# Optimization experiments

Hardware: AMD Instinct MI355X
Metric: run time of the kernel (lower is better)

The kernel has to match this reference:

```python
import jax, jax.numpy as jnp
import numpy as np

B, V, T, F = 1, 16, 1, 1
ZF, ZA, ZQ = 5, 4, 7
N = 12 * 4 ** ZF          # 12288 field nodes
n = 4 ** (ZQ - ZF)        # 16 packed channels per node (in_features_q)
K = 9                     # adjc.shape[-1], neighborhood size
ATT = 128                 # att_dim
H = 32                    # n_head_channels
NH = ATT // H             # 4 heads
NA = 4 ** (ZF - ZA)       # 4-node local attention window
MULT = 2


def _ln(x, s, b):
    m = jnp.mean(x, axis=-1, keepdims=True)
    v = jnp.mean((x - m) ** 2, axis=-1, keepdims=True)
    return (x - m) * jax.lax.rsqrt(v + 1e-5) * s + b


def setup_inputs() -> dict:
    key = jax.random.key(0)
    ks = jax.random.split(key, 8)
    d = {}
    d["x"] = jax.random.normal(ks[0], (B, V, T, N * n, F), jnp.float32)
    d["adjc"] = jax.random.randint(ks[1], (N, K), 0, N)
    d["ln1_scale"] = jnp.ones((n,), jnp.float32)
    d["ln1_bias"] = jnp.zeros((n,), jnp.float32)
    d["W_q"] = jax.random.normal(ks[2], (n, ATT), jnp.float32) / np.sqrt(n)
    d["W_kv"] = jax.random.normal(ks[3], (n * K, 2 * ATT), jnp.float32) / np.sqrt(n * K)
    d["b_kv"] = jnp.zeros((2 * ATT,), jnp.float32)
    d["W_out"] = jax.random.normal(ks[4], (ATT, n), jnp.float32) / np.sqrt(ATT)
    d["b_out"] = jnp.zeros((n,), jnp.float32)
    d["gamma"] = jnp.full((n,), 1e-6, jnp.float32)
    d["ln2_scale"] = jnp.ones((n,), jnp.float32)
    d["ln2_bias"] = jnp.zeros((n,), jnp.float32)
    d["W1"] = jax.random.normal(ks[5], (n, n * MULT), jnp.float32) / np.sqrt(n)
    d["b1"] = jnp.zeros((n * MULT,), jnp.float32)
    d["W2"] = jax.random.normal(ks[6], (n * MULT, n), jnp.float32) / np.sqrt(n * MULT)
    d["b2"] = jnp.zeros((n,), jnp.float32)
    d["gamma_mlp"] = jnp.full((n,), 1e-6, jnp.float32)
    return d


def _forward(x, adjc, ln1_scale, ln1_bias, W_q, W_kv, b_kv, W_out, b_out,
             gamma, ln2_scale, ln2_bias, W1, b1, W2, b2, gamma_mlp):
    fv = F * V
    Ng = N // NA
    # combine_zooms + 'b v t N n f -> b (f v) t N n'
    xc = x.reshape(B, V, T, N, n, F)
    q = jnp.transpose(xc, (0, 5, 1, 2, 3, 4)).reshape(B, fv, T, N, n)
    x_res = q
    # emb_layer_q: layer norm, identity linear (in == out features)
    q = _ln(q, ln1_scale, ln1_bias)
    kv = q  # self-attention: kv shares the normalized q
    # q projection (no bias) and local-window reshape
    qp = (q @ W_q).reshape(B, fv, T, Ng, NA, ATT)
    # neighborhood gather on kv (with_nh_field): [b,fv,t,N,K,n] -> [b,fv,t,N,K*n]
    kv_nh = kv[:, :, :, adjc, :].reshape(B, fv, T, N, K * n)
    kvp = (kv_nh @ W_kv + b_kv).reshape(B, fv, T, Ng, NA, 2 * ATT)
    k, v = jnp.split(kvp, 2, axis=-1)

    def to_att(z):
        # 'b fv t N NA (NH H) -> (b N t) NH (fv NA) H'  (with_var_att)
        z = z.reshape(B, fv, T, Ng, NA, NH, H)
        z = jnp.transpose(z, (0, 3, 2, 5, 1, 4, 6))
        return z.reshape(B * Ng * T, NH, fv * NA, H)

    qa, ka, va = to_att(qp), to_att(k), to_att(v)
    scores = jnp.einsum('znqh,znkh->znqk', qa, ka) / jnp.sqrt(jnp.asarray(H, qa.dtype))
    att = jax.nn.softmax(scores, axis=-1)
    out = jnp.einsum('znqk,znkh->znqh', att, va)
    # '(b N t) NH (fv NA) H -> b fv t (N NA) (NH H)'
    out = out.reshape(B, Ng, T, NH, fv, NA, H)
    out = jnp.transpose(out, (0, 4, 2, 1, 5, 3, 6)).reshape(B, fv, T, Ng * NA, NH * H)
    att_out = out @ W_out + b_out           # [b,fv,t,N,n]
    xo = x_res + gamma * att_out            # 'shift' update with gamma residual
    h = _ln(xo, ln2_scale, ln2_bias)        # mlp_emb_layer (identity linear)
    mlp = jax.nn.gelu(h @ W1 + b1) @ W2 + b2
    xo = xo + gamma_mlp * mlp
    # 'b (f v) t N n -> b v t (N n) f'
    y = xo.reshape(B, F, V, T, N, n)
    y = jnp.transpose(y, (0, 2, 3, 4, 5, 1)).reshape(B, V, T, N * n, F)
    return y


def reference(x, adjc, ln1_scale, ln1_bias, W_q, W_kv, b_kv, W_out, b_out,
              gamma, ln2_scale, ln2_bias, W1, b1, W2, b2, gamma_mlp):
    return _forward(x, adjc, ln1_scale, ln1_bias, W_q, W_kv, b_kv, W_out, b_out,
                    gamma, ln2_scale, ln2_bias, W1, b1, W2, b2, gamma_mlp)
```

## Files before the change

kernel.cpp:

```cpp
#include <hip/hip_runtime.h>
#include <math.h>

#define NNODE 12288
#define XSTRIDE 196608
#define NGRP 3072
#define XT_ELEMS 3145728
#define WS_WQT   0
#define WS_WKVT  4096
#define WS_WOUTT 45056
#define WS_W1T   47104
#define WS_W2T   48128
#define WS_WTOT  48640
#define WS_BYTES ((size_t)(XT_ELEMS + WS_WTOT) * 2)

typedef unsigned short u16;
typedef short short8 __attribute__((ext_vector_type(8)));
typedef float f32x4 __attribute__((ext_vector_type(4)));

#define MFMA16(a,b,c) __builtin_amdgcn_mfma_f32_16x16x32_bf16((a),(b),(c),0,0,0)

__device__ __forceinline__ u16 f2b(float f) {
  unsigned u = __float_as_uint(f);
  return (u16)((u + 0x7FFFu + ((u >> 16) & 1u)) >> 16);
}
__device__ __forceinline__ unsigned pk2(float a, float b) {
  return (__float_as_uint(a) >> 16) | (__float_as_uint(b) & 0xFFFF0000u);
}
__device__ __forceinline__ float gelu_fast(float v) {
  float u = v * (1.0f + 0.044715f * v * v);
  float e = __expf(-1.5957691216057308f * u);
  return v / (1.0f + e);
}
#define DS_FENCE() do { asm volatile("s_waitcnt lgkmcnt(0)" ::: "memory"); \
                        __builtin_amdgcn_sched_barrier(0); } while (0)

__device__ __forceinline__ float softmax16(f32x4 s4[4]) {
  const float C2 = 0.25508682300212037f;
  f32x4 m01, m23;
  #pragma unroll
  for (int r = 0; r < 4; ++r) { m01[r] = fmaxf(s4[0][r], s4[1][r]); m23[r] = fmaxf(s4[2][r], s4[3][r]); }
  float mx = fmaxf(fmaxf(fmaxf(m01[0], m23[0]), fmaxf(m01[1], m23[1])),
                   fmaxf(fmaxf(m01[2], m23[2]), fmaxf(m01[3], m23[3])));
  mx = fmaxf(mx, __shfl_xor(mx, 16));
  mx = fmaxf(mx, __shfl_xor(mx, 32));
  float nmx = mx * C2;
  float sum = 0.f;
  #pragma unroll
  for (int mt = 0; mt < 4; ++mt)
    #pragma unroll
    for (int r = 0; r < 4; ++r) {
      float e = exp2f(__builtin_fmaf(s4[mt][r], C2, -nmx));
      s4[mt][r] = e; sum += e;
    }
  sum += __shfl_xor(sum, 16);
  sum += __shfl_xor(sum, 32);
  return 1.0f / sum;
}

__global__ __launch_bounds__(256)
void ln1x_prep(const float* __restrict__ x, const float* __restrict__ ln1s,
               const float* __restrict__ ln1b,
               const float* __restrict__ Wq, const float* __restrict__ Wkv,
               const float* __restrict__ Wout, const float* __restrict__ W1,
               const float* __restrict__ W2, u16* __restrict__ ws)
{
  const int t = threadIdx.x;
  if (blockIdx.x >= 768) {
    int i = (blockIdx.x - 768) * 256 + t;
    if (i >= WS_WTOT) return;
    u16* wbase = ws + XT_ELEMS;
    int j = i;
    if (j < 4096)  { int n = j >> 5, k = j & 31;   wbase[WS_WQT   + j] = f2b(k < 16  ? Wq[k * 128 + n]  : 0.f); return; }
    j -= 4096;
    if (j < 40960) { int n = j / 160, k = j % 160; wbase[WS_WKVT  + j] = f2b(k < 144 ? Wkv[k * 256 + n] : 0.f); return; }
    j -= 40960;
    if (j < 2048)  { int n = j >> 7, k = j & 127;  wbase[WS_WOUTT + j] = f2b(Wout[k * 16 + n]); return; }
    j -= 2048;
    if (j < 1024)  { int n = j >> 5, k = j & 31;   wbase[WS_W1T   + j] = f2b(k < 16 ? W1[k * 32 + n] : 0.f); return; }
    j -= 1024;
    { int n = j >> 5, k = j & 31; wbase[WS_W2T + j] = f2b(W2[k * 16 + n]); }
    return;
  }
  __shared__ u16 buf[4096];
  const int node0 = blockIdx.x * 16;
  const int v = t >> 4, nd = t & 15;
  const f32x4* xp = (const f32x4*)(x + (size_t)v * XSTRIDE + (node0 + nd) * 16);
  f32x4 p0 = xp[0], p1 = xp[1], p2 = xp[2], p3 = xp[3];
  float va[16] = {p0[0],p0[1],p0[2],p0[3], p1[0],p1[1],p1[2],p1[3],
                  p2[0],p2[1],p2[2],p2[3], p3[0],p3[1],p3[2],p3[3]};
  float s = 0.f, ss = 0.f;
  #pragma unroll
  for (int j = 0; j < 16; ++j) { s += va[j]; ss += va[j] * va[j]; }
  float mean = s * 0.0625f, rs = rsqrtf(ss * 0.0625f - mean * mean + 1e-5f);
  short8 o0, o1;
  #pragma unroll
  for (int j = 0; j < 8; ++j) {
    o0[j] = (short)f2b((va[j]     - mean) * rs * ln1s[j]     + ln1b[j]);
    o1[j] = (short)f2b((va[j + 8] - mean) * rs * ln1s[j + 8] + ln1b[j + 8]);
  }
  *(short8*)(buf + nd * 256 + v * 16)     = o0;
  *(short8*)(buf + nd * 256 + v * 16 + 8) = o1;
  __syncthreads();
  const short8* src = (const short8*)(buf + t * 16);
  short8* dst = (short8*)(ws + node0 * 256 + t * 16);
  dst[0] = src[0]; dst[1] = src[1];
}

__global__ __launch_bounds__(256, 3)
void mfa_main(const float* __restrict__ x, const int* __restrict__ adjc,
              const float* __restrict__ bkv, const float* __restrict__ bout,
              const float* __restrict__ gamma, const float* __restrict__ ln2s,
              const float* __restrict__ ln2b, const float* __restrict__ b1,
              const float* __restrict__ b2, const float* __restrict__ gmlp,
              const u16* __restrict__ ws, float* __restrict__ y)
{
  __shared__ __align__(16) unsigned char smem[49152];
  const int t = threadIdx.x, g = blockIdx.x;
  const int w = t >> 6, lrow = t & 15, kgrp = (t >> 4) & 3, k0 = kgrp * 8;
  const int swzl = (lrow & 7) << 4;

  char* stage = (char*)smem;
  char* kbuf  = (char*)smem;
  char* vtb   = (char*)(smem + 16384);
  char* qps   = (char*)(smem + 32768 + w * 4096);

  const u16* xt = ws;
  const u16* wb = ws + XT_ELEMS;
  const f32x4 z4 = {0.f, 0.f, 0.f, 0.f};
  const short8 z8 = {0,0,0,0,0,0,0,0};

  int an[5], srow[5], scolb[5]; bool szp[5];
  #pragma unroll
  for (int p = 0; p < 5; ++p) {
    int j = p * 256 + t, s = j >> 5, half = j & 1, vv = (j & 31) >> 1;
    if (s < 36) { an[p] = adjc[g * 36 + s]; srow[p] = vv * 4 + (s / 9); scolb[p] = (s % 9) * 32 + half * 16; szp[p] = false; }
    else { srow[p] = (s - 36) * 16 + vv; scolb[p] = 288 + half * 16; szp[p] = true; an[p] = 0; }
  }
  short8 sv[5];
  #pragma unroll
  for (int p = 0; p < 5; ++p) {
    if (!szp[p]) { int j = p * 256 + t, vv = (j & 31) >> 1, half = j & 1;
                   sv[p] = *(const short8*)(xt + an[p] * 256 + vv * 16 + half * 8); }
    else sv[p] = z8;
  }
  const int tok = w * 16 + lrow, tv = tok >> 2, tnode = g * 4 + (lrow & 3);
  short8 qbx = (kgrp < 2) ? *(const short8*)(xt + tnode * 256 + tv * 16 + k0) : z8;
  #pragma unroll
  for (int p = 0; p < 5; ++p) *(short8*)(stage + srow[p] * 336 + scolb[p]) = sv[p];
  #pragma unroll
  for (int ft = 0; ft < 8; ++ft) {
    short8 wA = *(const short8*)(wb + WS_WQT + (ft * 16 + lrow) * 32 + k0);
    f32x4 c = MFMA16(wA, qbx, z4);
    *(uint2*)(qps + lrow * 256 + ((32 * ft + 8 * kgrp) ^ swzl)) =
        make_uint2(pk2(c[0], c[1]), pk2(c[2], c[3]));
  }
  __syncthreads();

  f32x4 acc[4][4];
  #pragma unroll
  for (int c = 0; c < 4; ++c)
    #pragma unroll
    for (int mt = 0; mt < 4; ++mt) acc[c][mt] = z4;
  const int ctk = 2 * w, ctv = 8 + 2 * w;
  #pragma unroll
  for (int kc = 0; kc < 5; ++kc) {
    short8 tf[4], wf[4];
    #pragma unroll
    for (int mt = 0; mt < 4; ++mt)
      tf[mt] = *(const short8*)(stage + (mt * 16 + lrow) * 336 + kc * 64 + kgrp * 16);
    wf[0] = *(const short8*)(wb + WS_WKVT + ((ctk    ) * 16 + lrow) * 160 + kc * 32 + k0);
    wf[1] = *(const short8*)(wb + WS_WKVT + ((ctk + 1) * 16 + lrow) * 160 + kc * 32 + k0);
    wf[2] = *(const short8*)(wb + WS_WKVT + ((ctv    ) * 16 + lrow) * 160 + kc * 32 + k0);
    wf[3] = *(const short8*)(wb + WS_WKVT + ((ctv + 1) * 16 + lrow) * 160 + kc * 32 + k0);
    #pragma unroll
    for (int mt = 0; mt < 4; ++mt) {
      acc[0][mt] = MFMA16(wf[0], tf[mt], acc[0][mt]);
      acc[1][mt] = MFMA16(wf[1], tf[mt], acc[1][mt]);
      acc[2][mt] = MFMA16(tf[mt], wf[2], acc[2][mt]);
      acc[3][mt] = MFMA16(tf[mt], wf[3], acc[3][mt]);
    }
  }
  __syncthreads();
  #pragma unroll
  for (int c = 0; c < 2; ++c) {
    const int ct = ctk + c;
    f32x4 bk = *(const f32x4*)(bkv + ct * 16 + 4 * kgrp);
    #pragma unroll
    for (int mt = 0; mt < 4; ++mt) {
      f32x4 a = acc[c][mt];
      *(uint2*)(kbuf + (mt * 16 + lrow) * 256 + ((32 * ct + 8 * kgrp) ^ swzl)) =
          make_uint2(pk2(a[0] + bk[0], a[1] + bk[1]), pk2(a[2] + bk[2], a[3] + bk[3]));
    }
  }
  #pragma unroll
  for (int c = 0; c < 2; ++c) {
    const int vc = (2 * w + c) * 16 + lrow;
    float bv = bkv[128 + vc];
    #pragma unroll
    for (int mt = 0; mt < 4; ++mt) {
      f32x4 a = acc[2 + c][mt];
      *(uint2*)(vtb + vc * 128 + ((32 * mt + 8 * kgrp) ^ swzl)) =
          make_uint2(pk2(a[0] + bv, a[1] + bv), pk2(a[2] + bv, a[3] + bv));
    }
  }
  __syncthreads();

  short8 qbh0 = *(const short8*)(qps + lrow * 256 + ((  0 + 16 * kgrp) ^ swzl));
  short8 qbh1 = *(const short8*)(qps + lrow * 256 + (( 64 + 16 * kgrp) ^ swzl));
  short8 qbh2 = z8, qbh3 = z8;
  f32x4 oacc[4][2];
  float invh[4];
  #pragma unroll
  for (int h = 0; h < 4; ++h) { oacc[h][0] = z4; oacc[h][1] = z4; }

  #pragma unroll
  for (int hp = 0; hp < 2; ++hp) {
    const int h0 = 2 * hp, h1 = h0 + 1;
    f32x4 s4a[4], s4b[4];
    #pragma unroll
    for (int mt = 0; mt < 4; ++mt) {
      short8 ka = *(const short8*)(kbuf + (mt * 16 + lrow) * 256 + ((64 * h0 + 16 * kgrp) ^ swzl));
      s4a[mt] = MFMA16(ka, hp ? qbh2 : qbh0, z4);
    }
    #pragma unroll
    for (int mt = 0; mt < 4; ++mt) {
      short8 kb = *(const short8*)(kbuf + (mt * 16 + lrow) * 256 + ((64 * h1 + 16 * kgrp) ^ swzl));
      s4b[mt] = MFMA16(kb, hp ? qbh3 : qbh1, z4);
    }
    if (hp == 0) {
      qbh2 = *(const short8*)(qps + lrow * 256 + ((128 + 16 * kgrp) ^ swzl));
      qbh3 = *(const short8*)(qps + lrow * 256 + ((192 + 16 * kgrp) ^ swzl));
    }
    invh[h0] = softmax16(s4a);
    invh[h1] = softmax16(s4b);
    #pragma unroll
    for (int mt = 0; mt < 4; ++mt) {
      *(uint2*)(qps + lrow * 256 + ((      32 * mt + 8 * kgrp) ^ swzl)) =
          make_uint2(pk2(s4a[mt][0], s4a[mt][1]), pk2(s4a[mt][2], s4a[mt][3]));
      *(uint2*)(qps + lrow * 256 + ((128 + 32 * mt + 8 * kgrp) ^ swzl)) =
          make_uint2(pk2(s4b[mt][0], s4b[mt][1]), pk2(s4b[mt][2], s4b[mt][3]));
    }
    DS_FENCE();
    #pragma unroll
    for (int hh = 0; hh < 2; ++hh) {
      const int h = 2 * hp + hh;
      #pragma unroll
      for (int kc = 0; kc < 2; ++kc) {
        short8 pB = *(const short8*)(qps + lrow * 256 + ((128 * hh + 64 * kc + 16 * kgrp) ^ swzl));
        #pragma unroll
        for (int nt = 0; nt < 2; ++nt) {
          short8 vA = *(const short8*)(vtb + (h * 32 + nt * 16 + lrow) * 128 + ((64 * kc + 16 * kgrp) ^ swzl));
          oacc[h][nt] = MFMA16(vA, pB, oacc[h][nt]);
        }
      }
    }
  }

  f32x4 p_gam = *(const f32x4*)(gamma + 4 * kgrp);
  f32x4 p_bo  = *(const f32x4*)(bout  + 4 * kgrp);
  f32x4 p_l2s = *(const f32x4*)(ln2s  + 4 * kgrp);
  f32x4 p_l2b = *(const f32x4*)(ln2b  + 4 * kgrp);
  f32x4 p_b1a = *(const f32x4*)(b1 + 4 * kgrp);
  f32x4 p_b1b = *(const f32x4*)(b1 + 16 + 4 * kgrp);
  f32x4 p_b2  = *(const f32x4*)(b2   + 4 * kgrp);
  f32x4 p_gm2 = *(const f32x4*)(gmlp + 4 * kgrp);
  f32x4 xr = *(const f32x4*)(x + (size_t)tv * XSTRIDE + tnode * 16 + 4 * kgrp);

  #pragma unroll
  for (int h = 0; h < 4; ++h) {
    float iv = invh[h];
    #pragma unroll
    for (int nt = 0; nt < 2; ++nt) {
      f32x4 a = oacc[h][nt];
      *(uint2*)(qps + lrow * 256 + ((64 * h + 32 * nt + 8 * kgrp) ^ swzl)) =
          make_uint2(pk2(a[0] * iv, a[1] * iv), pk2(a[2] * iv, a[3] * iv));
    }
  }
  DS_FENCE();

  f32x4 oc = z4;
  #pragma unroll
  for (int kc = 0; kc < 4; ++kc) {
    short8 oB = *(const short8*)(qps + lrow * 256 + ((64 * kc + 16 * kgrp) ^ swzl));
    short8 wo = *(const short8*)(wb + WS_WOUTT + lrow * 128 + kc * 32 + k0);
    oc = MFMA16(wo, oB, oc);
  }
  float xov[4]; float s = 0.f, ss = 0.f;
  #pragma unroll
  for (int r = 0; r < 4; ++r) {
    xov[r] = xr[r] + p_gam[r] * (oc[r] + p_bo[r]);
    s += xov[r]; ss += xov[r] * xov[r];
  }
  s  += __shfl_xor(s, 16);  s  += __shfl_xor(s, 32);
  ss += __shfl_xor(ss, 16); ss += __shfl_xor(ss, 32);
  float mean = s * 0.0625f, rstd = rsqrtf(ss * 0.0625f - mean * mean + 1e-5f);
  float hv[4];
  #pragma unroll
  for (int r = 0; r < 4; ++r) hv[r] = (xov[r] - mean) * rstd * p_l2s[r] + p_l2b[r];
  *(uint2*)(qps + lrow * 64 + 8 * kgrp)      = make_uint2(pk2(hv[0], hv[1]), pk2(hv[2], hv[3]));
  *(uint2*)(qps + lrow * 64 + 32 + 8 * kgrp) = make_uint2(0u, 0u);
  DS_FENCE();
  short8 hB = *(const short8*)(qps + lrow * 64 + 16 * kgrp);
  float hid[8];
  #pragma unroll
  for (int ft = 0; ft < 2; ++ft) {
    short8 w1 = *(const short8*)(wb + WS_W1T + (ft * 16 + lrow) * 32 + k0);
    f32x4 hc = MFMA16(w1, hB, z4);
    f32x4 bb = ft ? p_b1b : p_b1a;
    #pragma unroll
    for (int r = 0; r < 4; ++r) hid[ft * 4 + r] = gelu_fast(hc[r] + bb[r]);
  }
  *(uint2*)(qps + 2048 + lrow * 64 + 8 * kgrp)      = make_uint2(pk2(hid[0], hid[1]), pk2(hid[2], hid[3]));
  *(uint2*)(qps + 2048 + lrow * 64 + 32 + 8 * kgrp) = make_uint2(pk2(hid[4], hid[5]), pk2(hid[6], hid[7]));
  DS_FENCE();
  short8 hidB = *(const short8*)(qps + 2048 + lrow * 64 + 16 * kgrp);
  short8 w2 = *(const short8*)(wb + WS_W2T + lrow * 32 + k0);
  f32x4 mc = MFMA16(w2, hidB, z4);
  f32x4 yv;
  #pragma unroll
  for (int r = 0; r < 4; ++r) yv[r] = xov[r] + p_gm2[r] * (mc[r] + p_b2[r]);
  *(f32x4*)(y + (size_t)tv * XSTRIDE + tnode * 16 + 4 * kgrp) = yv;
}

extern "C" void kernel_launch(void* const* d_in, const int* in_sizes, int n_in,
                              void* d_out, int out_size, void* d_ws, size_t ws_size,
                              hipStream_t stream) {
  const float* x    = (const float*)d_in[0];
  const int*   adjc = (const int*)  d_in[1];
  const float* ln1s = (const float*)d_in[2];
  const float* ln1b = (const float*)d_in[3];
  const float* Wq   = (const float*)d_in[4];
  const float* Wkv  = (const float*)d_in[5];
  const float* bkv  = (const float*)d_in[6];
  const float* Wout = (const float*)d_in[7];
  const float* bout = (const float*)d_in[8];
  const float* gam  = (const float*)d_in[9];
  const float* ln2s = (const float*)d_in[10];
  const float* ln2b = (const float*)d_in[11];
  const float* W1   = (const float*)d_in[12];
  const float* b1   = (const float*)d_in[13];
  const float* W2   = (const float*)d_in[14];
  const float* b2   = (const float*)d_in[15];
  const float* gmlp = (const float*)d_in[16];
  float* y = (float*)d_out;
  u16* ws = (u16*)d_ws;
  if (ws_size < WS_BYTES) return;

  ln1x_prep<<<958, 256, 0, stream>>>(x, ln1s, ln1b, Wq, Wkv, Wout, W1, W2, ws);
  mfa_main<<<NGRP, 256, 0, stream>>>(x, adjc, bkv, bout, gam, ln2s, ln2b,
                                     b1, b2, gmlp, ws, y);
}
```

Before: 155.1 us.

## Load neighbor KV fragments directly from global and pad LDS instead of swizzling

```diff
diff --git a/kernel.cpp b/kernel.cpp
--- a/kernel.cpp
+++ b/kernel.cpp
@@ -12,6 +12,11 @@
 #define WS_W2T   48128
 #define WS_WTOT  48640
 #define WS_BYTES ((size_t)(XT_ELEMS + WS_WTOT) * 2)
+
+#define KBUF_OFF 0
+#define VTB_OFF  17408
+#define QSL_OFF  34816
+#define LDS_TOTAL 53248
 
 typedef unsigned short u16;
 typedef short short8 __attribute__((ext_vector_type(8)));
@@ -114,47 +119,33 @@
               const float* __restrict__ b2, const float* __restrict__ gmlp,
               const u16* __restrict__ ws, float* __restrict__ y)
 {
-  __shared__ __align__(16) unsigned char smem[49152];
+  __shared__ __align__(16) unsigned char smem[LDS_TOTAL];
   const int t = threadIdx.x, g = blockIdx.x;
   const int w = t >> 6, lrow = t & 15, kgrp = (t >> 4) & 3, k0 = kgrp * 8;
-  const int swzl = (lrow & 7) << 4;
-
-  char* stage = (char*)smem;
-  char* kbuf  = (char*)smem;
-  char* vtb   = (char*)(smem + 16384);
-  char* qps   = (char*)(smem + 32768 + w * 4096);
+
+  char* kbuf = (char*)(smem + KBUF_OFF);
+  char* vtb  = (char*)(smem + VTB_OFF);
+  char* qsl  = (char*)(smem + QSL_OFF + w * 4608);
 
   const u16* xt = ws;
   const u16* wb = ws + XT_ELEMS;
   const f32x4 z4 = {0.f, 0.f, 0.f, 0.f};
   const short8 z8 = {0,0,0,0,0,0,0,0};
 
-  int an[5], srow[5], scolb[5]; bool szp[5];
-  #pragma unroll
-  for (int p = 0; p < 5; ++p) {
-    int j = p * 256 + t, s = j >> 5, half = j & 1, vv = (j & 31) >> 1;
-    if (s < 36) { an[p] = adjc[g * 36 + s]; srow[p] = vv * 4 + (s / 9); scolb[p] = (s % 9) * 32 + half * 16; szp[p] = false; }
-    else { srow[p] = (s - 36) * 16 + vv; scolb[p] = 288 + half * 16; szp[p] = true; an[p] = 0; }
-  }
-  short8 sv[5];
-  #pragma unroll
-  for (int p = 0; p < 5; ++p) {
-    if (!szp[p]) { int j = p * 256 + t, vv = (j & 31) >> 1, half = j & 1;
-                   sv[p] = *(const short8*)(xt + an[p] * 256 + vv * 16 + half * 8); }
-    else sv[p] = z8;
-  }
   const int tok = w * 16 + lrow, tv = tok >> 2, tnode = g * 4 + (lrow & 3);
+  const int* arow = adjc + tnode * 9;
+  int4 a03 = *(const int4*)(arow);
+  int4 a47 = *(const int4*)(arow + 4);
+  int  a8  = arow[8];
   short8 qbx = (kgrp < 2) ? *(const short8*)(xt + tnode * 256 + tv * 16 + k0) : z8;
-  #pragma unroll
-  for (int p = 0; p < 5; ++p) *(short8*)(stage + srow[p] * 336 + scolb[p]) = sv[p];
+
   #pragma unroll
   for (int ft = 0; ft < 8; ++ft) {
     short8 wA = *(const short8*)(wb + WS_WQT + (ft * 16 + lrow) * 32 + k0);
     f32x4 c = MFMA16(wA, qbx, z4);
-    *(uint2*)(qps + lrow * 256 + ((32 * ft + 8 * kgrp) ^ swzl)) =
+    *(uint2*)(qsl + lrow * 272 + 32 * ft + 8 * kgrp) =
         make_uint2(pk2(c[0], c[1]), pk2(c[2], c[3]));
   }
-  __syncthreads();
 
   f32x4 acc[4][4];
   #pragma unroll
@@ -162,12 +153,23 @@
     #pragma unroll
     for (int mt = 0; mt < 4; ++mt) acc[c][mt] = z4;
   const int ctk = 2 * w, ctv = 8 + 2 * w;
+  const int hi = kgrp >> 1, hlo = (kgrp & 1) * 8;
   #pragma unroll
   for (int kc = 0; kc < 5; ++kc) {
+    int an;
+    if      (kc == 0) an = hi ? a03.y : a03.x;
+    else if (kc == 1) an = hi ? a03.w : a03.z;
+    else if (kc == 2) an = hi ? a47.y : a47.x;
+    else if (kc == 3) an = hi ? a47.w : a47.z;
+    else              an = a8;
+    const bool dead = (kc == 4) && (hi == 1);
     short8 tf[4], wf[4];
     #pragma unroll
-    for (int mt = 0; mt < 4; ++mt)
-      tf[mt] = *(const short8*)(stage + (mt * 16 + lrow) * 336 + kc * 64 + kgrp * 16);
+    for (int mt = 0; mt < 4; ++mt) {
+      int vv = mt * 4 + (lrow >> 2);
+      short8 ld = *(const short8*)(xt + an * 256 + vv * 16 + hlo);
+      tf[mt] = dead ? z8 : ld;
+    }
     wf[0] = *(const short8*)(wb + WS_WKVT + ((ctk    ) * 16 + lrow) * 160 + kc * 32 + k0);
     wf[1] = *(const short8*)(wb + WS_WKVT + ((ctk + 1) * 16 + lrow) * 160 + kc * 32 + k0);
     wf[2] = *(const short8*)(wb + WS_WKVT + ((ctv    ) * 16 + lrow) * 160 + kc * 32 + k0);
@@ -180,7 +182,6 @@
       acc[3][mt] = MFMA16(tf[mt], wf[3], acc[3][mt]);
     }
   }
-  __syncthreads();
   #pragma unroll
   for (int c = 0; c < 2; ++c) {
     const int ct = ctk + c;
@@ -188,7 +189,7 @@
     #pragma unroll
     for (int mt = 0; mt < 4; ++mt) {
       f32x4 a = acc[c][mt];
-      *(uint2*)(kbuf + (mt * 16 + lrow) * 256 + ((32 * ct + 8 * kgrp) ^ swzl)) =
+      *(uint2*)(kbuf + (mt * 16 + lrow) * 272 + 32 * ct + 8 * kgrp) =
           make_uint2(pk2(a[0] + bk[0], a[1] + bk[1]), pk2(a[2] + bk[2], a[3] + bk[3]));
     }
   }
@@ -199,14 +200,14 @@
     #pragma unroll
     for (int mt = 0; mt < 4; ++mt) {
       f32x4 a = acc[2 + c][mt];
-      *(uint2*)(vtb + vc * 128 + ((32 * mt + 8 * kgrp) ^ swzl)) =
+      *(uint2*)(vtb + vc * 136 + 32 * mt + 8 * kgrp) =
           make_uint2(pk2(a[0] + bv, a[1] + bv), pk2(a[2] + bv, a[3] + bv));
     }
   }
   __syncthreads();
 
-  short8 qbh0 = *(const short8*)(qps + lrow * 256 + ((  0 + 16 * kgrp) ^ swzl));
-  short8 qbh1 = *(const short8*)(qps + lrow * 256 + (( 64 + 16 * kgrp) ^ swzl));
+  short8 qbh0 = *(const short8*)(qsl + lrow * 272 +   0 + 16 * kgrp);
+  short8 qbh1 = *(const short8*)(qsl + lrow * 272 +  64 + 16 * kgrp);
   short8 qbh2 = z8, qbh3 = z8;
   f32x4 oacc[4][2];
   float invh[4];
@@ -219,25 +220,25 @@
     f32x4 s4a[4], s4b[4];
     #pragma unroll
     for (int mt = 0; mt < 4; ++mt) {
-      short8 ka = *(const short8*)(kbuf + (mt * 16 + lrow) * 256 + ((64 * h0 + 16 * kgrp) ^ swzl));
+      short8 ka = *(const short8*)(kbuf + (mt * 16 + lrow) * 272 + 64 * h0 + 16 * kgrp);
       s4a[mt] = MFMA16(ka, hp ? qbh2 : qbh0, z4);
     }
     #pragma unroll
     for (int mt = 0; mt < 4; ++mt) {
-      short8 kb = *(const short8*)(kbuf + (mt * 16 + lrow) * 256 + ((64 * h1 + 16 * kgrp) ^ swzl));
+      short8 kb = *(const short8*)(kbuf + (mt * 16 + lrow) * 272 + 64 * h1 + 16 * kgrp);
       s4b[mt] = MFMA16(kb, hp ? qbh3 : qbh1, z4);
     }
     if (hp == 0) {
-      qbh2 = *(const short8*)(qps + lrow * 256 + ((128 + 16 * kgrp) ^ swzl));
-      qbh3 = *(const short8*)(qps + lrow * 256 + ((192 + 16 * kgrp) ^ swzl));
+      qbh2 = *(const short8*)(qsl + lrow * 272 + 128 + 16 * kgrp);
+      qbh3 = *(const short8*)(qsl + lrow * 272 + 192 + 16 * kgrp);
     }
     invh[h0] = softmax16(s4a);
     invh[h1] = softmax16(s4b);
     #pragma unroll
     for (int mt = 0; mt < 4; ++mt) {
-      *(uint2*)(qps + lrow * 256 + ((      32 * mt + 8 * kgrp) ^ swzl)) =
+      *(uint2*)(qsl + lrow * 272 +       32 * mt + 8 * kgrp) =
           make_uint2(pk2(s4a[mt][0], s4a[mt][1]), pk2(s4a[mt][2], s4a[mt][3]));
-      *(uint2*)(qps + lrow * 256 + ((128 + 32 * mt + 8 * kgrp) ^ swzl)) =
+      *(uint2*)(qsl + lrow * 272 + 128 + 32 * mt + 8 * kgrp) =
           make_uint2(pk2(s4b[mt][0], s4b[mt][1]), pk2(s4b[mt][2], s4b[mt][3]));
     }
     DS_FENCE();
@@ -246,10 +247,10 @@
       const int h = 2 * hp + hh;
       #pragma unroll
       for (int kc = 0; kc < 2; ++kc) {
-        short8 pB = *(const short8*)(qps + lrow * 256 + ((128 * hh + 64 * kc + 16 * kgrp) ^ swzl));
+        short8 pB = *(const short8*)(qsl + lrow * 272 + 128 * hh + 64 * kc + 16 * kgrp);
         #pragma unroll
         for (int nt = 0; nt < 2; ++nt) {
-          short8 vA = *(const short8*)(vtb + (h * 32 + nt * 16 + lrow) * 128 + ((64 * kc + 16 * kgrp) ^ swzl));
+          short8 vA = *(const short8*)(vtb + (h * 32 + nt * 16 + lrow) * 136 + 64 * kc + 16 * kgrp);
           oacc[h][nt] = MFMA16(vA, pB, oacc[h][nt]);
         }
       }
@@ -272,7 +273,7 @@
     #pragma unroll
     for (int nt = 0; nt < 2; ++nt) {
       f32x4 a = oacc[h][nt];
-      *(uint2*)(qps + lrow * 256 + ((64 * h + 32 * nt + 8 * kgrp) ^ swzl)) =
+      *(uint2*)(qsl + lrow * 272 + 64 * h + 32 * nt + 8 * kgrp) =
           make_uint2(pk2(a[0] * iv, a[1] * iv), pk2(a[2] * iv, a[3] * iv));
     }
   }
@@ -281,7 +282,7 @@
   f32x4 oc = z4;
   #pragma unroll
   for (int kc = 0; kc < 4; ++kc) {
-    short8 oB = *(const short8*)(qps + lrow * 256 + ((64 * kc + 16 * kgrp) ^ swzl));
+    short8 oB = *(const short8*)(qsl + lrow * 272 + 64 * kc + 16 * kgrp);
     short8 wo = *(const short8*)(wb + WS_WOUTT + lrow * 128 + kc * 32 + k0);
     oc = MFMA16(wo, oB, oc);
   }
@@ -297,10 +298,10 @@
   float hv[4];
   #pragma unroll
   for (int r = 0; r < 4; ++r) hv[r] = (xov[r] - mean) * rstd * p_l2s[r] + p_l2b[r];
-  *(uint2*)(qps + lrow * 64 + 8 * kgrp)      = make_uint2(pk2(hv[0], hv[1]), pk2(hv[2], hv[3]));
-  *(uint2*)(qps + lrow * 64 + 32 + 8 * kgrp) = make_uint2(0u, 0u);
+  *(uint2*)(qsl + lrow * 144 + 8 * kgrp)      = make_uint2(pk2(hv[0], hv[1]), pk2(hv[2], hv[3]));
+  *(uint2*)(qsl + lrow * 144 + 32 + 8 * kgrp) = make_uint2(0u, 0u);
   DS_FENCE();
-  short8 hB = *(const short8*)(qps + lrow * 64 + 16 * kgrp);
+  short8 hB = *(const short8*)(qsl + lrow * 144 + 16 * kgrp);
   float hid[8];
   #pragma unroll
   for (int ft = 0; ft < 2; ++ft) {
@@ -310,10 +311,10 @@
     #pragma unroll
     for (int r = 0; r < 4; ++r) hid[ft * 4 + r] = gelu_fast(hc[r] + bb[r]);
   }
-  *(uint2*)(qps + 2048 + lrow * 64 + 8 * kgrp)      = make_uint2(pk2(hid[0], hid[1]), pk2(hid[2], hid[3]));
-  *(uint2*)(qps + 2048 + lrow * 64 + 32 + 8 * kgrp) = make_uint2(pk2(hid[4], hid[5]), pk2(hid[6], hid[7]));
+  *(uint2*)(qsl + lrow * 144 + 72 + 8 * kgrp)      = make_uint2(pk2(hid[0], hid[1]), pk2(hid[2], hid[3]));
+  *(uint2*)(qsl + lrow * 144 + 72 + 32 + 8 * kgrp) = make_uint2(pk2(hid[4], hid[5]), pk2(hid[6], hid[7]));
   DS_FENCE();
-  short8 hidB = *(const short8*)(qps + 2048 + lrow * 64 + 16 * kgrp);
+  short8 hidB = *(const short8*)(qsl + lrow * 144 + 72 + 16 * kgrp);
   short8 w2 = *(const short8*)(wb + WS_W2T + lrow * 32 + k0);
   f32x4 mc = MFMA16(w2, hidB, z4);
   f32x4 yv;
```

Result: slower. 178.2 us (+14.9%).

## Remap token order per wave and replace XOR swizzle with padded LDS strides

Applied to the files above, without the earlier changes.

```diff
diff --git a/kernel.cpp b/kernel.cpp
--- a/kernel.cpp
+++ b/kernel.cpp
@@ -12,6 +12,16 @@
 #define WS_W2T   48128
 #define WS_WTOT  48640
 #define WS_BYTES ((size_t)(XT_ELEMS + WS_WTOT) * 2)
+
+#define S_STAGE 336
+#define S_K     272
+#define S_VT    144
+#define S_Q     272
+#define KBUF_OFF 0
+#define VTB_OFF  17408
+#define QSL_OFF  35840
+#define QSL_SLOT 4608
+#define LDS_TOTAL 54272
 
 typedef unsigned short u16;
 typedef short short8 __attribute__((ext_vector_type(8)));
@@ -114,46 +124,52 @@
               const float* __restrict__ b2, const float* __restrict__ gmlp,
               const u16* __restrict__ ws, float* __restrict__ y)
 {
-  __shared__ __align__(16) unsigned char smem[49152];
+  __shared__ __align__(16) unsigned char smem[LDS_TOTAL];
   const int t = threadIdx.x, g = blockIdx.x;
   const int w = t >> 6, lrow = t & 15, kgrp = (t >> 4) & 3, k0 = kgrp * 8;
-  const int swzl = (lrow & 7) << 4;
 
   char* stage = (char*)smem;
-  char* kbuf  = (char*)smem;
-  char* vtb   = (char*)(smem + 16384);
-  char* qps   = (char*)(smem + 32768 + w * 4096);
+  char* kbuf  = (char*)(smem + KBUF_OFF);
+  char* vtb   = (char*)(smem + VTB_OFF);
+  char* qsl   = (char*)(smem + QSL_OFF + w * QSL_SLOT);
 
   const u16* xt = ws;
   const u16* wb = ws + XT_ELEMS;
   const f32x4 z4 = {0.f, 0.f, 0.f, 0.f};
   const short8 z8 = {0,0,0,0,0,0,0,0};
 
-  int an[5], srow[5], scolb[5]; bool szp[5];
+  const int tnode = g * 4 + w;
+
+  short8 qbx = (kgrp < 2) ? *(const short8*)(xt + tnode * 256 + lrow * 16 + k0) : z8;
+  short8 wqA[8];
+  #pragma unroll
+  for (int ft = 0; ft < 8; ++ft)
+    wqA[ft] = *(const short8*)(wb + WS_WQT + (ft * 16 + lrow) * 32 + k0);
+
+  int srow[5], scolb[5]; bool szp[5]; short8 sv[5];
   #pragma unroll
   for (int p = 0; p < 5; ++p) {
     int j = p * 256 + t, s = j >> 5, half = j & 1, vv = (j & 31) >> 1;
-    if (s < 36) { an[p] = adjc[g * 36 + s]; srow[p] = vv * 4 + (s / 9); scolb[p] = (s % 9) * 32 + half * 16; szp[p] = false; }
-    else { srow[p] = (s - 36) * 16 + vv; scolb[p] = 288 + half * 16; szp[p] = true; an[p] = 0; }
-  }
-  short8 sv[5];
-  #pragma unroll
-  for (int p = 0; p < 5; ++p) {
-    if (!szp[p]) { int j = p * 256 + t, vv = (j & 31) >> 1, half = j & 1;
-                   sv[p] = *(const short8*)(xt + an[p] * 256 + vv * 16 + half * 8); }
-    else sv[p] = z8;
-  }
-  const int tok = w * 16 + lrow, tv = tok >> 2, tnode = g * 4 + (lrow & 3);
-  short8 qbx = (kgrp < 2) ? *(const short8*)(xt + tnode * 256 + tv * 16 + k0) : z8;
-  #pragma unroll
-  for (int p = 0; p < 5; ++p) *(short8*)(stage + srow[p] * 336 + scolb[p]) = sv[p];
+    if (s < 36) {
+      int k = s >> 2, ni = s & 3;
+      int an = adjc[g * 36 + ni * 9 + k];
+      srow[p] = ni * 16 + vv; scolb[p] = k * 32 + half * 16; szp[p] = false;
+      sv[p] = *(const short8*)(xt + an * 256 + vv * 16 + half * 8);
+    } else {
+      int z = (s - 36) * 32 + (t & 31);
+      srow[p] = z >> 1; scolb[p] = 288 + (z & 1) * 16; szp[p] = true; sv[p] = z8;
+    }
+  }
+
   #pragma unroll
   for (int ft = 0; ft < 8; ++ft) {
-    short8 wA = *(const short8*)(wb + WS_WQT + (ft * 16 + lrow) * 32 + k0);
-    f32x4 c = MFMA16(wA, qbx, z4);
-    *(uint2*)(qps + lrow * 256 + ((32 * ft + 8 * kgrp) ^ swzl)) =
+    f32x4 c = MFMA16(wqA[ft], qbx, z4);
+    *(uint2*)(qsl + lrow * S_Q + 32 * ft + 8 * kgrp) =
         make_uint2(pk2(c[0], c[1]), pk2(c[2], c[3]));
   }
+  #pragma unroll
+  for (int p = 0; p < 5; ++p)
+    *(short8*)(stage + srow[p] * S_STAGE + scolb[p]) = sv[p];
   __syncthreads();
 
   f32x4 acc[4][4];
@@ -167,7 +183,7 @@
     short8 tf[4], wf[4];
     #pragma unroll
     for (int mt = 0; mt < 4; ++mt)
-      tf[mt] = *(const short8*)(stage + (mt * 16 + lrow) * 336 + kc * 64 + kgrp * 16);
+      tf[mt] = *(const short8*)(stage + (mt * 16 + lrow) * S_STAGE + kc * 64 + kgrp * 16);
     wf[0] = *(const short8*)(wb + WS_WKVT + ((ctk    ) * 16 + lrow) * 160 + kc * 32 + k0);
     wf[1] = *(const short8*)(wb + WS_WKVT + ((ctk + 1) * 16 + lrow) * 160 + kc * 32 + k0);
     wf[2] = *(const short8*)(wb + WS_WKVT + ((ctv    ) * 16 + lrow) * 160 + kc * 32 + k0);
@@ -188,7 +204,7 @@
     #pragma unroll
     for (int mt = 0; mt < 4; ++mt) {
       f32x4 a = acc[c][mt];
-      *(uint2*)(kbuf + (mt * 16 + lrow) * 256 + ((32 * ct + 8 * kgrp) ^ swzl)) =
+      *(uint2*)(kbuf + (mt * 16 + lrow) * S_K + 32 * ct + 8 * kgrp) =
           make_uint2(pk2(a[0] + bk[0], a[1] + bk[1]), pk2(a[2] + bk[2], a[3] + bk[3]));
     }
   }
@@ -199,14 +215,14 @@
     #pragma unroll
     for (int mt = 0; mt < 4; ++mt) {
       f32x4 a = acc[2 + c][mt];
-      *(uint2*)(vtb + vc * 128 + ((32 * mt + 8 * kgrp) ^ swzl)) =
+      *(uint2*)(vtb + vc * S_VT + 32 * mt + 8 * kgrp) =
           make_uint2(pk2(a[0] + bv, a[1] + bv), pk2(a[2] + bv, a[3] + bv));
     }
   }
   __syncthreads();
 
-  short8 qbh0 = *(const short8*)(qps + lrow * 256 + ((  0 + 16 * kgrp) ^ swzl));
-  short8 qbh1 = *(const short8*)(qps + lrow * 256 + (( 64 + 16 * kgrp) ^ swzl));
+  short8 qbh0 = *(const short8*)(qsl + lrow * S_Q +   0 + 16 * kgrp);
+  short8 qbh1 = *(const short8*)(qsl + lrow * S_Q +  64 + 16 * kgrp);
   short8 qbh2 = z8, qbh3 = z8;
   f32x4 oacc[4][2];
   float invh[4];
@@ -219,25 +235,25 @@
     f32x4 s4a[4], s4b[4];
     #pragma unroll
     for (int mt = 0; mt < 4; ++mt) {
-      short8 ka = *(const short8*)(kbuf + (mt * 16 + lrow) * 256 + ((64 * h0 + 16 * kgrp) ^ swzl));
+      short8 ka = *(const short8*)(kbuf + (mt * 16 + lrow) * S_K + 64 * h0 + 16 * kgrp);
       s4a[mt] = MFMA16(ka, hp ? qbh2 : qbh0, z4);
     }
     #pragma unroll
     for (int mt = 0; mt < 4; ++mt) {
-      short8 kb = *(const short8*)(kbuf + (mt * 16 + lrow) * 256 + ((64 * h1 + 16 * kgrp) ^ swzl));
+      short8 kb = *(const short8*)(kbuf + (mt * 16 + lrow) * S_K + 64 * h1 + 16 * kgrp);
       s4b[mt] = MFMA16(kb, hp ? qbh3 : qbh1, z4);
     }
     if (hp == 0) {
-      qbh2 = *(const short8*)(qps + lrow * 256 + ((128 + 16 * kgrp) ^ swzl));
-      qbh3 = *(const short8*)(qps + lrow * 256 + ((192 + 16 * kgrp) ^ swzl));
+      qbh2 = *(const short8*)(qsl + lrow * S_Q + 128 + 16 * kgrp);
+      qbh3 = *(const short8*)(qsl + lrow * S_Q + 192 + 16 * kgrp);
     }
     invh[h0] = softmax16(s4a);
     invh[h1] = softmax16(s4b);
     #pragma unroll
     for (int mt = 0; mt < 4; ++mt) {
-      *(uint2*)(qps + lrow * 256 + ((      32 * mt + 8 * kgrp) ^ swzl)) =
+      *(uint2*)(qsl + lrow * S_Q +       32 * mt + 8 * kgrp) =
           make_uint2(pk2(s4a[mt][0], s4a[mt][1]), pk2(s4a[mt][2], s4a[mt][3]));
-      *(uint2*)(qps + lrow * 256 + ((128 + 32 * mt + 8 * kgrp) ^ swzl)) =
+      *(uint2*)(qsl + lrow * S_Q + 128 + 32 * mt + 8 * kgrp) =
           make_uint2(pk2(s4b[mt][0], s4b[mt][1]), pk2(s4b[mt][2], s4b[mt][3]));
     }
     DS_FENCE();
@@ -246,10 +262,10 @@
       const int h = 2 * hp + hh;
       #pragma unroll
       for (int kc = 0; kc < 2; ++kc) {
-        short8 pB = *(const short8*)(qps + lrow * 256 + ((128 * hh + 64 * kc + 16 * kgrp) ^ swzl));
+        short8 pB = *(const short8*)(qsl + lrow * S_Q + 128 * hh + 64 * kc + 16 * kgrp);
         #pragma unroll
         for (int nt = 0; nt < 2; ++nt) {
-          short8 vA = *(const short8*)(vtb + (h * 32 + nt * 16 + lrow) * 128 + ((64 * kc + 16 * kgrp) ^ swzl));
+          short8 vA = *(const short8*)(vtb + (h * 32 + nt * 16 + lrow) * S_VT + 64 * kc + 16 * kgrp);
           oacc[h][nt] = MFMA16(vA, pB, oacc[h][nt]);
         }
       }
@@ -264,7 +280,7 @@
   f32x4 p_b1b = *(const f32x4*)(b1 + 16 + 4 * kgrp);
   f32x4 p_b2  = *(const f32x4*)(b2   + 4 * kgrp);
   f32x4 p_gm2 = *(const f32x4*)(gmlp + 4 * kgrp);
-  f32x4 xr = *(const f32x4*)(x + (size_t)tv * XSTRIDE + tnode * 16 + 4 * kgrp);
+  f32x4 xr = *(const f32x4*)(x + (size_t)lrow * XSTRIDE + tnode * 16 + 4 * kgrp);
 
   #pragma unroll
   for (int h = 0; h < 4; ++h) {
@@ -272,7 +288,7 @@
     #pragma unroll
     for (int nt = 0; nt < 2; ++nt) {
       f32x4 a = oacc[h][nt];
-      *(uint2*)(qps + lrow * 256 + ((64 * h + 32 * nt + 8 * kgrp) ^ swzl)) =
+      *(uint2*)(qsl + lrow * S_Q + 64 * h + 32 * nt + 8 * kgrp) =
           make_uint2(pk2(a[0] * iv, a[1] * iv), pk2(a[2] * iv, a[3] * iv));
     }
   }
@@ -281,7 +297,7 @@
   f32x4 oc = z4;
   #pragma unroll
   for (int kc = 0; kc < 4; ++kc) {
-    short8 oB = *(const short8*)(qps + lrow * 256 + ((64 * kc + 16 * kgrp) ^ swzl));
+    short8 oB = *(const short8*)(qsl + lrow * S_Q + 64 * kc + 16 * kgrp);
     short8 wo = *(const short8*)(wb + WS_WOUTT + lrow * 128 + kc * 32 + k0);
     oc = MFMA16(wo, oB, oc);
   }
@@ -297,10 +313,10 @@
   float hv[4];
   #pragma unroll
   for (int r = 0; r < 4; ++r) hv[r] = (xov[r] - mean) * rstd * p_l2s[r] + p_l2b[r];
-  *(uint2*)(qps + lrow * 64 + 8 * kgrp)      = make_uint2(pk2(hv[0], hv[1]), pk2(hv[2], hv[3]));
-  *(uint2*)(qps + lrow * 64 + 32 + 8 * kgrp) = make_uint2(0u, 0u);
+  *(uint2*)(qsl + lrow * S_VT + 8 * kgrp)      = make_uint2(pk2(hv[0], hv[1]), pk2(hv[2], hv[3]));
+  *(uint2*)(qsl + lrow * S_VT + 32 + 8 * kgrp) = make_uint2(0u, 0u);
   DS_FENCE();
-  short8 hB = *(const short8*)(qps + lrow * 64 + 16 * kgrp);
+  short8 hB = *(const short8*)(qsl + lrow * S_VT + 16 * kgrp);
   float hid[8];
   #pragma unroll
   for (int ft = 0; ft < 2; ++ft) {
@@ -310,16 +326,16 @@
     #pragma unroll
     for (int r = 0; r < 4; ++r) hid[ft * 4 + r] = gelu_fast(hc[r] + bb[r]);
   }
-  *(uint2*)(qps + 2048 + lrow * 64 + 8 * kgrp)      = make_uint2(pk2(hid[0], hid[1]), pk2(hid[2], hid[3]));
-  *(uint2*)(qps + 2048 + lrow * 64 + 32 + 8 * kgrp) = make_uint2(pk2(hid[4], hid[5]), pk2(hid[6], hid[7]));
+  *(uint2*)(qsl + 2304 + lrow * S_VT + 8 * kgrp)      = make_uint2(pk2(hid[0], hid[1]), pk2(hid[2], hid[3]));
+  *(uint2*)(qsl + 2304 + lrow * S_VT + 32 + 8 * kgrp) = make_uint2(pk2(hid[4], hid[5]), pk2(hid[6], hid[7]));
   DS_FENCE();
-  short8 hidB = *(const short8*)(qps + 2048 + lrow * 64 + 16 * kgrp);
+  short8 hidB = *(const short8*)(qsl + 2304 + lrow * S_VT + 16 * kgrp);
   short8 w2 = *(const short8*)(wb + WS_W2T + lrow * 32 + k0);
   f32x4 mc = MFMA16(w2, hidB, z4);
   f32x4 yv;
   #pragma unroll
   for (int r = 0; r < 4; ++r) yv[r] = xov[r] + p_gm2[r] * (mc[r] + p_b2[r]);
-  *(f32x4*)(y + (size_t)tv * XSTRIDE + tnode * 16 + 4 * kgrp) = yv;
+  *(f32x4*)(y + (size_t)lrow * XSTRIDE + tnode * 16 + 4 * kgrp) = yv;
 }
 
 extern "C" void kernel_launch(void* const* d_in, const int* in_sizes, int n_in,
```

Result: slower. 169.0 us (+8.9%).
